# Kernel tuning notes

Hardware: AMD Instinct MI355X
Metric: run time of the kernel (lower is better)

Reference implementation:

```python
import jax, jax.numpy as jnp
import numpy as np

EPS = 1e-5
NEG_SLOPE = 0.2


def setup_inputs() -> dict:
    key = jax.random.key(0)
    ks = jax.random.split(key, 8)
    N, E = 100000, 1600000
    x = jax.random.normal(ks[0], (N, 256), dtype=jnp.float32)
    adj_row = jnp.sort(jax.random.randint(ks[1], (E,), 0, N, dtype=jnp.int32))
    adj_col = jax.random.randint(ks[2], (E,), 0, N, dtype=jnp.int32)
    adj_vals = jax.random.uniform(ks[3], (E,), dtype=jnp.float32)
    # xavier_uniform-style scale
    def xavier(k, fan_in, fan_out):
        lim = float(np.sqrt(6.0 / (fan_in + fan_out)))
        return jax.random.uniform(k, (fan_in, fan_out), minval=-lim, maxval=lim, dtype=jnp.float32)
    W1 = xavier(ks[4], 256, 128)
    W2 = xavier(ks[5], 128, 128)
    W3 = xavier(ks[6], 128, 64)
    W4 = xavier(ks[7], 64, 32)
    return {"x": x, "adj_row": adj_row, "adj_col": adj_col, "adj_vals": adj_vals,
            "W1": W1, "W2": W2, "W3": W3, "W4": W4}


def _gnn_layer(h, row, col, vals, W, n_nodes):
    # support = h @ W ; out = spmm(adj, support) ; leaky_relu
    support = h @ W                          # [N, out]
    msg = support[col] * vals[:, None]       # [E, out] gather + scale
    agg = jax.ops.segment_sum(msg, row, num_segments=n_nodes)
    return jax.nn.leaky_relu(agg, NEG_SLOPE)


def _bn(h):
    # BatchNorm1d(affine=False, track_running_stats=False): batch stats, biased var
    mean = jnp.mean(h, axis=0)
    var = jnp.var(h, axis=0)
    return (h - mean) * jax.lax.rsqrt(var + EPS)


def reference(x, adj_row, adj_col, adj_vals, W1, W2, W3, W4):
    n = x.shape[0]
    h1 = _bn(jax.nn.elu(_gnn_layer(x, adj_row, adj_col, adj_vals, W1, n)))
    h2 = _bn(jax.nn.elu(_gnn_layer(h1, adj_row, adj_col, adj_vals, W2, n)))
    h3 = _bn(jax.nn.elu(_gnn_layer(h2, adj_row, adj_col, adj_vals, W3, n)))
    h4 = _bn(jax.nn.elu(_gnn_layer(h3, adj_row, adj_col, adj_vals, W4, n)))
    return (h1, h2, h3, h4)
```

## Files before the change

### kernel.cpp

```cpp
#include <hip/hip_runtime.h>
#include <hip/hip_bf16.h>

typedef __attribute__((ext_vector_type(8))) short short8;
typedef __attribute__((ext_vector_type(4))) float floatx4;
typedef __attribute__((ext_vector_type(8))) unsigned short ushortx8;

__device__ __forceinline__ float b2f(unsigned short u) {
    return __uint_as_float(((unsigned int)u) << 16);
}
__device__ __forceinline__ unsigned short f2b(float f) {
    __hip_bfloat16 b = __float2bfloat16(f);
    return *(unsigned short*)&b;
}
__device__ __forceinline__ float act_elu_lrelu(float x) {
    return x >= 0.f ? x : expm1f(0.2f * x);
}

__global__ void build_rowptr(const int* __restrict__ row, int* __restrict__ rp,
                             int E, int N) {
    int e = blockIdx.x * blockDim.x + threadIdx.x;
    if (e >= E) return;
    int r = row[e];
    int rprev = (e == 0) ? -1 : row[e - 1];
    for (int q = rprev + 1; q <= r; ++q) rp[q] = e;
    if (e == E - 1) {
        for (int q = r + 1; q <= N; ++q) rp[q] = E;
    }
}

__global__ __launch_bounds__(256) void wprep(
    const float* __restrict__ W1, const float* __restrict__ W2,
    const float* __restrict__ W3, const float* __restrict__ W4,
    unsigned short* __restrict__ B1, unsigned short* __restrict__ B2,
    unsigned short* __restrict__ B3, unsigned short* __restrict__ B4) {
    int i = blockIdx.x * 256 + threadIdx.x;
    const float* W;
    unsigned short* Wb;
    int CIN, COUT, idx;
    if (i < 32768) {
        W = W1; Wb = B1; CIN = 256; COUT = 128; idx = i;
    } else if (i < 49152) {
        W = W2; Wb = B2; CIN = 128; COUT = 128; idx = i - 32768;
    } else if (i < 57344) {
        W = W3; Wb = B3; CIN = 128; COUT = 64; idx = i - 49152;
    } else if (i < 59392) {
        W = W4; Wb = B4; CIN = 64; COUT = 32; idx = i - 57344;
    } else {
        return;
    }
    int k = idx / COUT, n = idx % COUT;
    int kc = k >> 3, kr = k & 7;
    Wb[((size_t)n * (CIN / 8) + (kc ^ (n & 7))) * 8 + kr] =
        (unsigned short)f2b(W[idx]);
}

template <int CIN, int COUT, bool NORM>
__global__ __launch_bounds__(256) void gemm_mfma(
    float* H, const unsigned short* __restrict__ Wb,
    unsigned short* __restrict__ S, const float* __restrict__ st, float invN,
    int Nrows) {
    __shared__ short Wt[CIN * COUT];
    constexpr int NCHUNK = CIN / 8;
    {
        constexpr int CHUNKS = CIN * COUT * 2 / 16;
        const short8* src = (const short8*)Wb;
        short8* dst = (short8*)Wt;
        for (int i = threadIdx.x; i < CHUNKS; i += 256) dst[i] = src[i];
    }
    __syncthreads();

    int wave = threadIdx.x >> 6, lane = threadIdx.x & 63;
    int m = lane & 15, quad = lane >> 4;
    int r0 = blockIdx.x * 64 + wave * 16;
    int rowi = r0 + m;
    int rowc = rowi < Nrows ? rowi : (Nrows - 1);

    short8 a[CIN / 32];
    const float* hrow = H + (size_t)rowc * CIN;
#pragma unroll
    for (int ks = 0; ks < CIN / 32; ++ks) {
        int c0 = ks * 32 + quad * 8;
        const float* p = hrow + c0;
        floatx4 x0 = *(const floatx4*)p;
        floatx4 x1 = *(const floatx4*)(p + 4);
        if constexpr (NORM) {
            floatx4 s0 = *(const floatx4*)(st + c0);
            floatx4 s1 = *(const floatx4*)(st + c0 + 4);
            floatx4 q0 = *(const floatx4*)(st + CIN + c0);
            floatx4 q1 = *(const floatx4*)(st + CIN + c0 + 4);
#pragma unroll
            for (int j = 0; j < 4; ++j) {
                float mean = s0[j] * invN;
                float var = q0[j] * invN - mean * mean;
                x0[j] = (x0[j] - mean) * rsqrtf(fmaxf(var, 0.f) + 1e-5f);
                mean = s1[j] * invN;
                var = q1[j] * invN - mean * mean;
                x1[j] = (x1[j] - mean) * rsqrtf(fmaxf(var, 0.f) + 1e-5f);
            }
            if (rowi < Nrows) {
                float* op = H + (size_t)rowi * CIN + c0;
                __builtin_nontemporal_store(x0, (floatx4*)op);
                __builtin_nontemporal_store(x1, (floatx4*)(op + 4));
            }
        }
        short8 t;
#pragma unroll
        for (int j = 0; j < 4; ++j) {
            t[j] = (short)f2b(x0[j]);
            t[4 + j] = (short)f2b(x1[j]);
        }
        a[ks] = t;
    }

#pragma unroll
    for (int nt = 0; nt < COUT / 16; ++nt) {
        floatx4 acc = {0.f, 0.f, 0.f, 0.f};
        int n = nt * 16 + m;
#pragma unroll
        for (int ks = 0; ks < CIN / 32; ++ks) {
            int kc = ks * 4 + quad;
            short8 b = *(const short8*)(&Wt[((size_t)n * NCHUNK + (kc ^ (n & 7))) * 8]);
            acc = __builtin_amdgcn_mfma_f32_16x16x32_bf16(a[ks], b, acc, 0, 0, 0);
        }
#pragma unroll
        for (int reg = 0; reg < 4; ++reg) {
            int rr = r0 + quad * 4 + reg;
            if (rr < Nrows) S[(size_t)rr * COUT + n] = f2b(acc[reg]);
        }
    }
}

template <int C>
__global__ __launch_bounds__(256) void spmm_act_stats(
    const ushortx8* __restrict__ S8, const int* __restrict__ colIdx,
    const float* __restrict__ vals, const int* __restrict__ rowPtr,
    float* __restrict__ Ag, float* __restrict__ stats, int N) {
    constexpr int LPN = C / 8;
    constexpr int NPB = 256 / LPN;
    int sub = threadIdx.x / LPN;
    int lc = threadIdx.x % LPN;

    float s[8], s2[8];
#pragma unroll
    for (int j = 0; j < 8; ++j) { s[j] = 0.f; s2[j] = 0.f; }

    int ngroups = (N + NPB - 1) / NPB;
    for (int g = blockIdx.x; g < ngroups; g += gridDim.x) {
        int node = g * NPB + sub;
        if (node < N) {
            int e0 = rowPtr[node], e1 = rowPtr[node + 1];
            float acc[8];
#pragma unroll
            for (int j = 0; j < 8; ++j) acc[j] = 0.f;
            int e = e0;
            for (; e + 4 <= e1; e += 4) {
                int i0 = colIdx[e], i1 = colIdx[e + 1];
                int i2 = colIdx[e + 2], i3 = colIdx[e + 3];
                float v0 = vals[e], v1 = vals[e + 1];
                float v2 = vals[e + 2], v3 = vals[e + 3];
                ushortx8 g0 = S8[(size_t)i0 * LPN + lc];
                ushortx8 g1 = S8[(size_t)i1 * LPN + lc];
                ushortx8 g2 = S8[(size_t)i2 * LPN + lc];
                ushortx8 g3 = S8[(size_t)i3 * LPN + lc];
#pragma unroll
                for (int j = 0; j < 8; ++j)
                    acc[j] += v0 * b2f(g0[j]) + v1 * b2f(g1[j]) +
                              v2 * b2f(g2[j]) + v3 * b2f(g3[j]);
            }
            for (; e < e1; ++e) {
                int i0 = colIdx[e];
                float v0 = vals[e];
                ushortx8 g0 = S8[(size_t)i0 * LPN + lc];
#pragma unroll
                for (int j = 0; j < 8; ++j) acc[j] += v0 * b2f(g0[j]);
            }
            floatx4 r0, r1;
#pragma unroll
            for (int j = 0; j < 4; ++j) {
                float a0 = act_elu_lrelu(acc[j]);
                float a1 = act_elu_lrelu(acc[4 + j]);
                r0[j] = a0;
                r1[j] = a1;
                s[j] += a0;
                s2[j] += a0 * a0;
                s[4 + j] += a1;
                s2[4 + j] += a1 * a1;
            }
            float* op = Ag + (size_t)node * C + lc * 8;
            *(floatx4*)op = r0;
            *(floatx4*)(op + 4) = r1;
        }
    }

    __shared__ float sh[2][NPB][C];
#pragma unroll
    for (int j = 0; j < 8; ++j) {
        sh[0][sub][lc * 8 + j] = s[j];
        sh[1][sub][lc * 8 + j] = s2[j];
    }
    __syncthreads();
    if (threadIdx.x < C) {
        int c = threadIdx.x;
        float t0 = 0.f, t1 = 0.f;
#pragma unroll 4
        for (int gg = 0; gg < NPB; ++gg) {
            t0 += sh[0][gg][c];
            t1 += sh[1][gg][c];
        }
        atomicAdd(&stats[c], t0);
        atomicAdd(&stats[C + c], t1);
    }
}

template <int C>
__global__ __launch_bounds__(256) void bn_norm(
    float* __restrict__ Ag, const float* __restrict__ stats, int N) {
    constexpr int RPB = 256 / C;
    int c = threadIdx.x % C;
    int rg = threadIdx.x / C;
    float invN = 1.f / (float)N;
    float mean = stats[c] * invN;
    float var = stats[C + c] * invN - mean * mean;
    float inv = rsqrtf(fmaxf(var, 0.f) + 1e-5f);
    for (int r = blockIdx.x * RPB + rg; r < N; r += gridDim.x * RPB) {
        float x = Ag[(size_t)r * C + c];
        Ag[(size_t)r * C + c] = (x - mean) * inv;
    }
}

extern "C" void kernel_launch(void* const* d_in, const int* in_sizes, int n_in,
                              void* d_out, int out_size, void* d_ws,
                              size_t ws_size, hipStream_t stream) {
    const float* x = (const float*)d_in[0];
    const int* adj_row = (const int*)d_in[1];
    const int* adj_col = (const int*)d_in[2];
    const float* adj_vals = (const float*)d_in[3];
    const float* W1 = (const float*)d_in[4];
    const float* W2 = (const float*)d_in[5];
    const float* W3 = (const float*)d_in[6];
    const float* W4 = (const float*)d_in[7];

    int N = in_sizes[0] / 256;
    int E = in_sizes[1];

    char* ws = (char*)d_ws;
    int* rp = (int*)ws;
    size_t off = (((size_t)(N + 1) * 4) + 255) & ~(size_t)255;
    float* stats = (float*)(ws + off);
    off += 4 * 256 * sizeof(float);
    unsigned short* Wb1 = (unsigned short*)(ws + off); off += 32768 * 2;
    unsigned short* Wb2 = (unsigned short*)(ws + off); off += 16384 * 2;
    unsigned short* Wb3 = (unsigned short*)(ws + off); off += 8192 * 2;
    unsigned short* Wb4 = (unsigned short*)(ws + off); off += 2048 * 2;
    off = (off + 255) & ~(size_t)255;
    unsigned short* S = (unsigned short*)(ws + off);

    hipMemsetAsync(stats, 0, 4 * 256 * sizeof(float), stream);
    build_rowptr<<<(E + 255) / 256, 256, 0, stream>>>(adj_row, rp, E, N);
    wprep<<<232, 256, 0, stream>>>(W1, W2, W3, W4, Wb1, Wb2, Wb3, Wb4);

    float* h1 = (float*)d_out;
    float* h2 = h1 + (size_t)N * 128;
    float* h3 = h2 + (size_t)N * 128;
    float* h4 = h3 + (size_t)N * 64;

    float invN = 1.f / (float)N;
    int gblk = (N + 63) / 64;
    auto sgrid = [](int N, int npb) {
        int ng = (N + npb - 1) / npb;
        return ng < 2048 ? ng : 2048;
    };

    gemm_mfma<256, 128, false><<<gblk, 256, 0, stream>>>(
        (float*)x, Wb1, S, nullptr, invN, N);
    spmm_act_stats<128><<<sgrid(N, 16), 256, 0, stream>>>(
        (const ushortx8*)S, adj_col, adj_vals, rp, h1, stats + 0, N);

    gemm_mfma<128, 128, true><<<gblk, 256, 0, stream>>>(
        h1, Wb2, S, stats + 0, invN, N);
    spmm_act_stats<128><<<sgrid(N, 16), 256, 0, stream>>>(
        (const ushortx8*)S, adj_col, adj_vals, rp, h2, stats + 256, N);

    gemm_mfma<128, 64, true><<<gblk, 256, 0, stream>>>(
        h2, Wb3, S, stats + 256, invN, N);
    spmm_act_stats<64><<<sgrid(N, 32), 256, 0, stream>>>(
        (const ushortx8*)S, adj_col, adj_vals, rp, h3, stats + 512, N);

    gemm_mfma<64, 32, true><<<gblk, 256, 0, stream>>>(
        h3, Wb4, S, stats + 512, invN, N);
    spmm_act_stats<32><<<sgrid(N, 64), 256, 0, stream>>>(
        (const ushortx8*)S, adj_col, adj_vals, rp, h4, stats + 768, N);
    bn_norm<32><<<256, 256, 0, stream>>>(h4, stats + 768, N);
}
```

Before: 652.4 us.

## Split GEMM weights into LDS halves, deepen SpMM gather unroll, move stats to LDS

The GEMM kernel now runs 512 threads per block covering 128 rows. It stages only half of the bf16 weight matrix in LDS at a time, looping over two column halves with barriers in between, to cut LDS footprint and raise occupancy. The SpMM kernel adds an 8-edge unrolled gather loop to keep more loads in flight. It also keeps the per-thread BN stats in shared memory instead of registers, under an occupancy hint of 8. Index math switches from size_t to 32-bit ints. The trade-off is extra barriers, an extra weight reload per block, and LDS read-modify-write traffic per node.

```diff
diff --git a/kernel.cpp b/kernel.cpp
--- a/kernel.cpp
+++ b/kernel.cpp
@@ -55,28 +55,22 @@
 }
 
 template <int CIN, int COUT, bool NORM>
-__global__ __launch_bounds__(256) void gemm_mfma(
+__global__ __launch_bounds__(512, 8) void gemm_mfma(
     float* H, const unsigned short* __restrict__ Wb,
     unsigned short* __restrict__ S, const float* __restrict__ st, float invN,
     int Nrows) {
-    __shared__ short Wt[CIN * COUT];
+    constexpr int CHALF = COUT / 2;
     constexpr int NCHUNK = CIN / 8;
-    {
-        constexpr int CHUNKS = CIN * COUT * 2 / 16;
-        const short8* src = (const short8*)Wb;
-        short8* dst = (short8*)Wt;
-        for (int i = threadIdx.x; i < CHUNKS; i += 256) dst[i] = src[i];
-    }
-    __syncthreads();
+    __shared__ short Wt[CIN * CHALF];
 
     int wave = threadIdx.x >> 6, lane = threadIdx.x & 63;
     int m = lane & 15, quad = lane >> 4;
-    int r0 = blockIdx.x * 64 + wave * 16;
+    int r0 = blockIdx.x * 128 + wave * 16;
     int rowi = r0 + m;
     int rowc = rowi < Nrows ? rowi : (Nrows - 1);
 
     short8 a[CIN / 32];
-    const float* hrow = H + (size_t)rowc * CIN;
+    const float* hrow = H + rowc * CIN;
 #pragma unroll
     for (int ks = 0; ks < CIN / 32; ++ks) {
         int c0 = ks * 32 + quad * 8;
@@ -98,7 +92,7 @@
                 x1[j] = (x1[j] - mean) * rsqrtf(fmaxf(var, 0.f) + 1e-5f);
             }
             if (rowi < Nrows) {
-                float* op = H + (size_t)rowi * CIN + c0;
+                float* op = H + rowi * CIN + c0;
                 __builtin_nontemporal_store(x0, (floatx4*)op);
                 __builtin_nontemporal_store(x1, (floatx4*)(op + 4));
             }
@@ -113,36 +107,53 @@
     }
 
 #pragma unroll
-    for (int nt = 0; nt < COUT / 16; ++nt) {
-        floatx4 acc = {0.f, 0.f, 0.f, 0.f};
-        int n = nt * 16 + m;
-#pragma unroll
-        for (int ks = 0; ks < CIN / 32; ++ks) {
-            int kc = ks * 4 + quad;
-            short8 b = *(const short8*)(&Wt[((size_t)n * NCHUNK + (kc ^ (n & 7))) * 8]);
-            acc = __builtin_amdgcn_mfma_f32_16x16x32_bf16(a[ks], b, acc, 0, 0, 0);
-        }
-#pragma unroll
-        for (int reg = 0; reg < 4; ++reg) {
-            int rr = r0 + quad * 4 + reg;
-            if (rr < Nrows) S[(size_t)rr * COUT + n] = f2b(acc[reg]);
-        }
+    for (int h = 0; h < 2; ++h) {
+        {
+            constexpr int CHUNKS = CIN * CHALF / 8;
+            const short8* src = (const short8*)(Wb + h * CIN * CHALF);
+            short8* dst = (short8*)Wt;
+            for (int i = threadIdx.x; i < CHUNKS; i += 512) dst[i] = src[i];
+        }
+        __syncthreads();
+
+#pragma unroll
+        for (int nt = 0; nt < CHALF / 16; ++nt) {
+            floatx4 acc = {0.f, 0.f, 0.f, 0.f};
+            int nn = nt * 16 + m;
+#pragma unroll
+            for (int ks = 0; ks < CIN / 32; ++ks) {
+                int kc = ks * 4 + quad;
+                short8 b =
+                    *(const short8*)(&Wt[(nn * NCHUNK + (kc ^ (nn & 7))) * 8]);
+                acc = __builtin_amdgcn_mfma_f32_16x16x32_bf16(a[ks], b, acc, 0,
+                                                              0, 0);
+            }
+            int n = h * CHALF + nn;
+#pragma unroll
+            for (int reg = 0; reg < 4; ++reg) {
+                int rr = r0 + quad * 4 + reg;
+                if (rr < Nrows) S[rr * COUT + n] = f2b(acc[reg]);
+            }
+        }
+        __syncthreads();
     }
 }
 
 template <int C>
-__global__ __launch_bounds__(256) void spmm_act_stats(
+__global__ __launch_bounds__(256, 8) void spmm_act_stats(
     const ushortx8* __restrict__ S8, const int* __restrict__ colIdx,
     const float* __restrict__ vals, const int* __restrict__ rowPtr,
     float* __restrict__ Ag, float* __restrict__ stats, int N) {
     constexpr int LPN = C / 8;
     constexpr int NPB = 256 / LPN;
+    __shared__ float sh[NPB][2][C];
     int sub = threadIdx.x / LPN;
     int lc = threadIdx.x % LPN;
 
-    float s[8], s2[8];
-#pragma unroll
-    for (int j = 0; j < 8; ++j) { s[j] = 0.f; s2[j] = 0.f; }
+    float* st0 = &sh[sub][0][lc * 8];
+    float* st1 = &sh[sub][1][lc * 8];
+#pragma unroll
+    for (int j = 0; j < 8; ++j) { st0[j] = 0.f; st1[j] = 0.f; }
 
     int ngroups = (N + NPB - 1) / NPB;
     for (int g = blockIdx.x; g < ngroups; g += gridDim.x) {
@@ -153,15 +164,39 @@
 #pragma unroll
             for (int j = 0; j < 8; ++j) acc[j] = 0.f;
             int e = e0;
+            for (; e + 8 <= e1; e += 8) {
+                int i0 = colIdx[e], i1 = colIdx[e + 1];
+                int i2 = colIdx[e + 2], i3 = colIdx[e + 3];
+                int i4 = colIdx[e + 4], i5 = colIdx[e + 5];
+                int i6 = colIdx[e + 6], i7 = colIdx[e + 7];
+                float v0 = vals[e], v1 = vals[e + 1];
+                float v2 = vals[e + 2], v3 = vals[e + 3];
+                float v4 = vals[e + 4], v5 = vals[e + 5];
+                float v6 = vals[e + 6], v7 = vals[e + 7];
+                ushortx8 g0 = S8[i0 * LPN + lc];
+                ushortx8 g1 = S8[i1 * LPN + lc];
+                ushortx8 g2 = S8[i2 * LPN + lc];
+                ushortx8 g3 = S8[i3 * LPN + lc];
+                ushortx8 g4 = S8[i4 * LPN + lc];
+                ushortx8 g5 = S8[i5 * LPN + lc];
+                ushortx8 g6 = S8[i6 * LPN + lc];
+                ushortx8 g7 = S8[i7 * LPN + lc];
+#pragma unroll
+                for (int j = 0; j < 8; ++j)
+                    acc[j] += v0 * b2f(g0[j]) + v1 * b2f(g1[j]) +
+                              v2 * b2f(g2[j]) + v3 * b2f(g3[j]) +
+                              v4 * b2f(g4[j]) + v5 * b2f(g5[j]) +
+                              v6 * b2f(g6[j]) + v7 * b2f(g7[j]);
+            }
             for (; e + 4 <= e1; e += 4) {
                 int i0 = colIdx[e], i1 = colIdx[e + 1];
                 int i2 = colIdx[e + 2], i3 = colIdx[e + 3];
                 float v0 = vals[e], v1 = vals[e + 1];
                 float v2 = vals[e + 2], v3 = vals[e + 3];
-                ushortx8 g0 = S8[(size_t)i0 * LPN + lc];
-                ushortx8 g1 = S8[(size_t)i1 * LPN + lc];
-                ushortx8 g2 = S8[(size_t)i2 * LPN + lc];
-                ushortx8 g3 = S8[(size_t)i3 * LPN + lc];
+                ushortx8 g0 = S8[i0 * LPN + lc];
+                ushortx8 g1 = S8[i1 * LPN + lc];
+                ushortx8 g2 = S8[i2 * LPN + lc];
+                ushortx8 g3 = S8[i3 * LPN + lc];
 #pragma unroll
                 for (int j = 0; j < 8; ++j)
                     acc[j] += v0 * b2f(g0[j]) + v1 * b2f(g1[j]) +
@@ -170,7 +205,7 @@
             for (; e < e1; ++e) {
                 int i0 = colIdx[e];
                 float v0 = vals[e];
-                ushortx8 g0 = S8[(size_t)i0 * LPN + lc];
+                ushortx8 g0 = S8[i0 * LPN + lc];
 #pragma unroll
                 for (int j = 0; j < 8; ++j) acc[j] += v0 * b2f(g0[j]);
             }
@@ -181,31 +216,25 @@
                 float a1 = act_elu_lrelu(acc[4 + j]);
                 r0[j] = a0;
                 r1[j] = a1;
-                s[j] += a0;
-                s2[j] += a0 * a0;
-                s[4 + j] += a1;
-                s2[4 + j] += a1 * a1;
-            }
-            float* op = Ag + (size_t)node * C + lc * 8;
+                st0[j] += a0;
+                st1[j] += a0 * a0;
+                st0[4 + j] += a1;
+                st1[4 + j] += a1 * a1;
+            }
+            float* op = Ag + node * C + lc * 8;
             *(floatx4*)op = r0;
             *(floatx4*)(op + 4) = r1;
         }
     }
 
-    __shared__ float sh[2][NPB][C];
-#pragma unroll
-    for (int j = 0; j < 8; ++j) {
-        sh[0][sub][lc * 8 + j] = s[j];
-        sh[1][sub][lc * 8 + j] = s2[j];
-    }
     __syncthreads();
     if (threadIdx.x < C) {
         int c = threadIdx.x;
         float t0 = 0.f, t1 = 0.f;
 #pragma unroll 4
         for (int gg = 0; gg < NPB; ++gg) {
-            t0 += sh[0][gg][c];
-            t1 += sh[1][gg][c];
+            t0 += sh[gg][0][c];
+            t1 += sh[gg][1][c];
         }
         atomicAdd(&stats[c], t0);
         atomicAdd(&stats[C + c], t1);
@@ -265,28 +294,28 @@
     float* h4 = h3 + (size_t)N * 64;
 
     float invN = 1.f / (float)N;
-    int gblk = (N + 63) / 64;
+    int gblk = (N + 127) / 128;
     auto sgrid = [](int N, int npb) {
         int ng = (N + npb - 1) / npb;
         return ng < 2048 ? ng : 2048;
     };
 
-    gemm_mfma<256, 128, false><<<gblk, 256, 0, stream>>>(
+    gemm_mfma<256, 128, false><<<gblk, 512, 0, stream>>>(
         (float*)x, Wb1, S, nullptr, invN, N);
     spmm_act_stats<128><<<sgrid(N, 16), 256, 0, stream>>>(
         (const ushortx8*)S, adj_col, adj_vals, rp, h1, stats + 0, N);
 
-    gemm_mfma<128, 128, true><<<gblk, 256, 0, stream>>>(
+    gemm_mfma<128, 128, true><<<gblk, 512, 0, stream>>>(
         h1, Wb2, S, stats + 0, invN, N);
     spmm_act_stats<128><<<sgrid(N, 16), 256, 0, stream>>>(
         (const ushortx8*)S, adj_col, adj_vals, rp, h2, stats + 256, N);
 
-    gemm_mfma<128, 64, true><<<gblk, 256, 0, stream>>>(
+    gemm_mfma<128, 64, true><<<gblk, 512, 0, stream>>>(
         h2, Wb3, S, stats + 256, invN, N);
     spmm_act_stats<64><<<sgrid(N, 32), 256, 0, stream>>>(
         (const ushortx8*)S, adj_col, adj_vals, rp, h3, stats + 512, N);
 
-    gemm_mfma<64, 32, true><<<gblk, 256, 0, stream>>>(
+    gemm_mfma<64, 32, true><<<gblk, 512, 0, stream>>>(
         h3, Wb4, S, stats + 512, invN, N);
     spmm_act_stats<32><<<sgrid(N, 64), 256, 0, stream>>>(
         (const ushortx8*)S, adj_col, adj_vals, rp, h4, stats + 768, N);
```

Result: slower. 762.7 us (+16.9%).

## Pipeline SpMM gathers through LDS with async global_load_lds double buffering

Applied to the files above, without the earlier changes.

The SpMM kernel now processes each node's edges in wave-uniform batches of four. It prefetches column indices two batches ahead and issues direct global-to-LDS 16-byte loads into a double-buffered per-wave stage, with explicit vmcnt waits and sched barriers so gathers overlap accumulation. Padded edges are clamped and their weight zeroed. Separately, the GEMM loads the weight matrix into LDS in two halves, which cuts shared memory per block and may raise occupancy at the cost of extra barriers. Risks include fragile hand-set waitcnt counts and wasted work when degrees differ within a wave.

```diff
diff --git a/kernel.cpp b/kernel.cpp
--- a/kernel.cpp
+++ b/kernel.cpp
@@ -15,6 +15,18 @@
 __device__ __forceinline__ float act_elu_lrelu(float x) {
     return x >= 0.f ? x : expm1f(0.2f * x);
 }
+
+__device__ __forceinline__ void gload16(const void* g, void* l) {
+    __builtin_amdgcn_global_load_lds(
+        (__attribute__((address_space(1))) void*)(g),
+        (__attribute__((address_space(3))) void*)(l), 16, 0, 0);
+}
+#define SB() __builtin_amdgcn_sched_barrier(0)
+#define WAITVM12()                                       \
+    do {                                                 \
+        asm volatile("s_waitcnt vmcnt(12)" ::: "memory"); \
+        __builtin_amdgcn_sched_barrier(0);               \
+    } while (0)
 
 __global__ void build_rowptr(const int* __restrict__ row, int* __restrict__ rp,
                              int E, int N) {
@@ -59,15 +71,9 @@
     float* H, const unsigned short* __restrict__ Wb,
     unsigned short* __restrict__ S, const float* __restrict__ st, float invN,
     int Nrows) {
-    __shared__ short Wt[CIN * COUT];
+    constexpr int CHALF = COUT / 2;
     constexpr int NCHUNK = CIN / 8;
-    {
-        constexpr int CHUNKS = CIN * COUT * 2 / 16;
-        const short8* src = (const short8*)Wb;
-        short8* dst = (short8*)Wt;
-        for (int i = threadIdx.x; i < CHUNKS; i += 256) dst[i] = src[i];
-    }
-    __syncthreads();
+    __shared__ short Wt[CIN * CHALF];
 
     int wave = threadIdx.x >> 6, lane = threadIdx.x & 63;
     int m = lane & 15, quad = lane >> 4;
@@ -113,20 +119,35 @@
     }
 
 #pragma unroll
-    for (int nt = 0; nt < COUT / 16; ++nt) {
-        floatx4 acc = {0.f, 0.f, 0.f, 0.f};
-        int n = nt * 16 + m;
-#pragma unroll
-        for (int ks = 0; ks < CIN / 32; ++ks) {
-            int kc = ks * 4 + quad;
-            short8 b = *(const short8*)(&Wt[((size_t)n * NCHUNK + (kc ^ (n & 7))) * 8]);
-            acc = __builtin_amdgcn_mfma_f32_16x16x32_bf16(a[ks], b, acc, 0, 0, 0);
-        }
-#pragma unroll
-        for (int reg = 0; reg < 4; ++reg) {
-            int rr = r0 + quad * 4 + reg;
-            if (rr < Nrows) S[(size_t)rr * COUT + n] = f2b(acc[reg]);
-        }
+    for (int h = 0; h < 2; ++h) {
+        {
+            constexpr int CHUNKS = CIN * CHALF / 8;
+            const short8* src = (const short8*)(Wb + h * CIN * CHALF);
+            short8* dst = (short8*)Wt;
+            for (int i = threadIdx.x; i < CHUNKS; i += 256) dst[i] = src[i];
+        }
+        __syncthreads();
+
+#pragma unroll
+        for (int nt = 0; nt < CHALF / 16; ++nt) {
+            floatx4 acc = {0.f, 0.f, 0.f, 0.f};
+            int nn = nt * 16 + m;
+#pragma unroll
+            for (int ks = 0; ks < CIN / 32; ++ks) {
+                int kc = ks * 4 + quad;
+                short8 b =
+                    *(const short8*)(&Wt[(nn * NCHUNK + (kc ^ (nn & 7))) * 8]);
+                acc = __builtin_amdgcn_mfma_f32_16x16x32_bf16(a[ks], b, acc, 0,
+                                                              0, 0);
+            }
+            int n = h * CHALF + nn;
+#pragma unroll
+            for (int reg = 0; reg < 4; ++reg) {
+                int rr = r0 + quad * 4 + reg;
+                if (rr < Nrows) S[(size_t)rr * COUT + n] = f2b(acc[reg]);
+            }
+        }
+        __syncthreads();
     }
 }
 
@@ -137,8 +158,14 @@
     float* __restrict__ Ag, float* __restrict__ stats, int N) {
     constexpr int LPN = C / 8;
     constexpr int NPB = 256 / LPN;
-    int sub = threadIdx.x / LPN;
-    int lc = threadIdx.x % LPN;
+    __shared__ char stage[4 * 2 * 4096];
+
+    int tid = threadIdx.x;
+    int sub = tid / LPN;
+    int lc = tid % LPN;
+    int wave = tid >> 6;
+    int lane = tid & 63;
+    char* wbase = stage + wave * 8192;
 
     float s[8], s2[8];
 #pragma unroll
@@ -147,33 +174,78 @@
     int ngroups = (N + NPB - 1) / NPB;
     for (int g = blockIdx.x; g < ngroups; g += gridDim.x) {
         int node = g * NPB + sub;
+        int nc = node < N ? node : N - 1;
+        int e0 = rowPtr[nc];
+        int e1 = node < N ? rowPtr[nc + 1] : e0;
+        int len = e1 - e0;
+        int wl = len;
+#pragma unroll
+        for (int mm = LPN; mm < 64; mm <<= 1) {
+            int o = __shfl_xor(wl, mm, 64);
+            wl = o > wl ? o : wl;
+        }
+        int tmax = (wl + 3) >> 2;
+        if (tmax == 0) continue;
+
+        auto ce = [&](int i) {
+            int q = i < e1 - 1 ? i : e1 - 1;
+            return q > 0 ? q : 0;
+        };
+
+        float acc[8];
+#pragma unroll
+        for (int j = 0; j < 8; ++j) acc[j] = 0.f;
+
+        int c0t[4];
+#pragma unroll
+        for (int k = 0; k < 4; ++k) c0t[k] = colIdx[ce(e0 + k)];
+        SB();
+        int ca[4];
+#pragma unroll
+        for (int k = 0; k < 4; ++k) ca[k] = colIdx[ce(e0 + 4 + k)];
+        SB();
+#pragma unroll
+        for (int k = 0; k < 4; ++k)
+            gload16(&S8[(size_t)c0t[k] * LPN + lc], wbase + k * 1024);
+        SB();
+        float vc[4];
+#pragma unroll
+        for (int k = 0; k < 4; ++k) vc[k] = vals[ce(e0 + k)];
+        SB();
+
+        for (int t = 0; t < tmax; ++t) {
+            int slot = t & 1;
+            int cb[4];
+            int b2 = e0 + t * 4 + 8;
+#pragma unroll
+            for (int k = 0; k < 4; ++k) cb[k] = colIdx[ce(b2 + k)];
+            SB();
+            WAITVM12();
+            char* dst = wbase + (slot ^ 1) * 4096;
+#pragma unroll
+            for (int k = 0; k < 4; ++k)
+                gload16(&S8[(size_t)ca[k] * LPN + lc], dst + k * 1024);
+            SB();
+            float vn[4];
+            int b1 = e0 + t * 4 + 4;
+#pragma unroll
+            for (int k = 0; k < 4; ++k) vn[k] = vals[ce(b1 + k)];
+            SB();
+            WAITVM12();
+            const char* src = wbase + slot * 4096 + lane * 16;
+            int b0 = e0 + t * 4;
+#pragma unroll
+            for (int k = 0; k < 4; ++k) {
+                ushortx8 gk = *(const ushortx8*)(src + k * 1024);
+                float v = (b0 + k < e1) ? vc[k] : 0.f;
+#pragma unroll
+                for (int j = 0; j < 8; ++j) acc[j] += v * b2f(gk[j]);
+            }
+#pragma unroll
+            for (int k = 0; k < 4; ++k) { ca[k] = cb[k]; vc[k] = vn[k]; }
+        }
+
         if (node < N) {
-            int e0 = rowPtr[node], e1 = rowPtr[node + 1];
-            float acc[8];
-#pragma unroll
-            for (int j = 0; j < 8; ++j) acc[j] = 0.f;
-            int e = e0;
-            for (; e + 4 <= e1; e += 4) {
-                int i0 = colIdx[e], i1 = colIdx[e + 1];
-                int i2 = colIdx[e + 2], i3 = colIdx[e + 3];
-                float v0 = vals[e], v1 = vals[e + 1];
-                float v2 = vals[e + 2], v3 = vals[e + 3];
-                ushortx8 g0 = S8[(size_t)i0 * LPN + lc];
-                ushortx8 g1 = S8[(size_t)i1 * LPN + lc];
-                ushortx8 g2 = S8[(size_t)i2 * LPN + lc];
-                ushortx8 g3 = S8[(size_t)i3 * LPN + lc];
-#pragma unroll
-                for (int j = 0; j < 8; ++j)
-                    acc[j] += v0 * b2f(g0[j]) + v1 * b2f(g1[j]) +
-                              v2 * b2f(g2[j]) + v3 * b2f(g3[j]);
-            }
-            for (; e < e1; ++e) {
-                int i0 = colIdx[e];
-                float v0 = vals[e];
-                ushortx8 g0 = S8[(size_t)i0 * LPN + lc];
-#pragma unroll
-                for (int j = 0; j < 8; ++j) acc[j] += v0 * b2f(g0[j]);
-            }
             floatx4 r0, r1;
 #pragma unroll
             for (int j = 0; j < 4; ++j) {
@@ -192,23 +264,22 @@
         }
     }
 
-    __shared__ float sh[2][NPB][C];
+    __syncthreads();
+    float* sh = (float*)stage;
 #pragma unroll
     for (int j = 0; j < 8; ++j) {
-        sh[0][sub][lc * 8 + j] = s[j];
-        sh[1][sub][lc * 8 + j] = s2[j];
+        sh[(0 * NPB + sub) * C + lc * 8 + j] = s[j];
+        sh[(1 * NPB + sub) * C + lc * 8 + j] = s2[j];
     }
     __syncthreads();
-    if (threadIdx.x < C) {
-        int c = threadIdx.x;
+    if (tid < C) {
         float t0 = 0.f, t1 = 0.f;
-#pragma unroll 4
         for (int gg = 0; gg < NPB; ++gg) {
-            t0 += sh[0][gg][c];
-            t1 += sh[1][gg][c];
-        }
-        atomicAdd(&stats[c], t0);
-        atomicAdd(&stats[C + c], t1);
+            t0 += sh[(0 * NPB + gg) * C + tid];
+            t1 += sh[(1 * NPB + gg) * C + tid];
+        }
+        atomicAdd(&stats[tid], t0);
+        atomicAdd(&stats[C + tid], t1);
     }
 }
 
```

Result: faster. 607.5 us (-6.9%).
